# Kernel optimization log

Hardware: AMD Instinct MI355X
Metric: run time of the kernel (lower is better)

## Reference

```python
import jax, jax.numpy as jnp
import numpy as np

N_NODES = 256
DIM = 128
N_LAYERS = 3
LN_EPS = 1e-5


def setup_inputs() -> dict:
    key = jax.random.key(0)
    ks = jax.random.split(key, 8)
    B = 2048
    node_features = jax.random.normal(ks[0], (B, N_NODES, DIM), dtype=jnp.float32)
    A_logits_pos = jax.random.normal(ks[1], (N_NODES, N_NODES), dtype=jnp.float32) * 0.01
    A_logits_neg = jax.random.normal(ks[2], (N_NODES, N_NODES), dtype=jnp.float32) * 0.01
    # per-layer Linear weights, torch layout (out_dim, in_dim); all dims are 128
    scale = 1.0 / np.sqrt(DIM)
    W_pos = jax.random.uniform(ks[3], (N_LAYERS, DIM, DIM), jnp.float32, -scale, scale)
    W_neg = jax.random.uniform(ks[4], (N_LAYERS, DIM, DIM), jnp.float32, -scale, scale)
    ln_g = jnp.ones((N_LAYERS, DIM), jnp.float32)
    ln_b = jnp.zeros((N_LAYERS, DIM), jnp.float32)
    ro_g = jnp.ones((DIM,), jnp.float32)
    ro_b = jnp.zeros((DIM,), jnp.float32)
    return {"node_features": node_features, "A_logits_pos": A_logits_pos,
            "A_logits_neg": A_logits_neg, "W_pos": W_pos, "W_neg": W_neg,
            "ln_g": ln_g, "ln_b": ln_b, "ro_g": ro_g, "ro_b": ro_b}


def _layernorm(x, g, b):
    mu = jnp.mean(x, axis=-1, keepdims=True)
    var = jnp.var(x, axis=-1, keepdims=True)
    return (x - mu) * jax.lax.rsqrt(var + LN_EPS) * g + b


def reference(node_features, A_logits_pos, A_logits_neg, W_pos, W_neg, ln_g, ln_b, ro_g, ro_b):
    # soft signed adjacency with hard-mask split (mask is non-differentiable)
    A_p = jax.nn.sigmoid(A_logits_pos)
    A_n = jax.nn.sigmoid(A_logits_neg)
    mask = (A_p > A_n).astype(A_p.dtype)
    A_pos = A_p * mask
    A_neg = A_n * (1.0 - mask)

    H = node_features  # (B, N, D)
    for l in range(N_LAYERS):
        agg_pos = jnp.einsum('uv,bvd->bud', A_pos, H)
        agg_neg = jnp.einsum('uv,bvd->bud', A_neg, H)
        # torch Linear: x @ W.T ; GELU is exact (erf) by default in torch
        out = jax.nn.gelu(jnp.einsum('bud,od->buo', agg_pos, W_pos[l])
                          - jnp.einsum('bud,od->buo', agg_neg, W_neg[l]),
                          approximate=False)
        H = _layernorm(out, ln_g[l], ln_b[l])  # dropout = identity in eval

    h_G = jnp.mean(H, axis=1)  # (B, D) readout
    return _layernorm(h_G, ro_g, ro_b)
```

## Files before the change

### kernel.cpp

```cpp
#include <hip/hip_runtime.h>
#include <math.h>


typedef float  f32x4  __attribute__((ext_vector_type(4)));
typedef float  f32x16 __attribute__((ext_vector_type(16)));
typedef short  s16x8  __attribute__((ext_vector_type(8)));
typedef __bf16 bf16x8 __attribute__((ext_vector_type(8)));

#define GOFF 65536

__device__ __forceinline__ unsigned short f2bf(float f) {
  unsigned int u = __builtin_bit_cast(unsigned int, f);
  u = (u + 0x7fffu + ((u >> 16) & 1u)) >> 16;
  return (unsigned short)u;
}
__device__ __forceinline__ float bf2f(unsigned short h) {
  return __builtin_bit_cast(float, (unsigned int)h << 16);
}

__device__ __forceinline__ int haddr(int v, int d) {
  return v * 256 + ((d * 2) ^ ((v & 15) << 4));
}
__device__ __forceinline__ int gaddr(int o, int vr) {
  return GOFF + o * 80 + vr * 2;
}

#define MFMA32(a, b, c) __builtin_amdgcn_mfma_f32_32x32x16_bf16( \
    __builtin_bit_cast(bf16x8, (a)), __builtin_bit_cast(bf16x8, (b)), (c), 0, 0, 0)

__global__ void prep_kernel(const float* __restrict__ alp, const float* __restrict__ aln,
                            const float* __restrict__ wp,  const float* __restrict__ wn,
                            unsigned short* __restrict__ A3, unsigned short* __restrict__ W3) {
  int idx = blockIdx.x * 512 + threadIdx.x;
  if (idx < 131072) {
    int j = idx & 7, lane = (idx >> 3) & 63, vt = (idx >> 9) & 15,
        ut = (idx >> 13) & 7, h = (idx >> 16) & 1;
    int u = ut * 32 + (lane & 31);
    int v = vt * 16 + (lane >> 5) * 8 + j;
    int s = u * 256 + v;
    float ap = 1.f / (1.f + expf(-alp[s]));
    float an = 1.f / (1.f + expf(-aln[s]));
    bool  m  = ap > an;
    float val = h ? (m ? 0.f : -an) : (m ? ap : 0.f);
    A3[idx] = f2bf(val);
  } else {
    int k = idx - 131072;
    int j = k & 7, lane = (k >> 3) & 63, kt = (k >> 9) & 7,
        ot = (k >> 12) & 3, hw = (k >> 14);
    int o = ot * 32 + (lane & 31);
    int d = kt * 16 + (lane >> 5) * 8 + j;
    const float* src = (hw & 1) ? wn : wp;
    W3[k] = f2bf(src[(hw >> 1) * 16384 + o * 128 + d]);
  }
}

__global__ __launch_bounds__(256, 2) void gnn_kernel(
    const float* __restrict__ X,
    const unsigned short* __restrict__ A3,
    const unsigned short* __restrict__ W3,
    const float* __restrict__ ln_g, const float* __restrict__ ln_b,
    const float* __restrict__ ro_g, const float* __restrict__ ro_b,
    float* __restrict__ out) {
  extern __shared__ char smem[];
  const int tid  = threadIdx.x;
  const int wid  = tid >> 6;
  const int lane = tid & 63;
  const int l31  = lane & 31;
  const int hi   = lane >> 5;
  const int b    = blockIdx.x;

  {
    const float4* Xb = (const float4*)(X + (size_t)b * 256 * 128);
#pragma unroll 8
    for (int i = 0; i < 32; ++i) {
      int idx = tid + i * 256;
      int v = idx >> 5, d = (idx & 31) * 4;
      float4 f = Xb[idx];
      ushort4 p;
      p.x = f2bf(f.x); p.y = f2bf(f.y); p.z = f2bf(f.z); p.w = f2bf(f.w);
      *(ushort4*)(smem + haddr(v, d)) = p;
    }
  }
  __syncthreads();

  f32x16 acc[2][4];
  for (int l = 0; l < 3; ++l) {
#pragma unroll
    for (int mt = 0; mt < 2; ++mt)
#pragma unroll
      for (int nt = 0; nt < 4; ++nt)
#pragma unroll
        for (int r = 0; r < 16; ++r) acc[mt][nt][r] = 0.f;

    for (int h = 0; h < 2; ++h) {
      const unsigned short* Wb = W3 + (size_t)(((l * 2 + h) * 4 + wid) * 8) * 512;
      const unsigned short* Ab = A3 + (size_t)((h * 8 + wid * 2) * 16) * 512;

      s16x8 wreg[8];
#pragma unroll
      for (int kt = 0; kt < 8; ++kt)
        wreg[kt] = *(const s16x8*)(Wb + (size_t)kt * 512 + lane * 8);

      for (int c = 0; c < 8; ++c) {
        f32x16 g0;
#pragma unroll
        for (int r = 0; r < 16; ++r) g0[r] = 0.f;
        const int v0 = c * 32 + l31;
#pragma unroll
        for (int kt = 0; kt < 8; ++kt) {
          s16x8 ha = *(const s16x8*)(smem + haddr(v0, kt * 16 + hi * 8));
          g0 = MFMA32(ha, wreg[kt], g0);
        }
        __syncthreads();
        {
          const int og = wid * 32 + l31;
#pragma unroll
          for (int rq = 0; rq < 4; ++rq) {
            int vr = rq * 8 + hi * 4;
            ushort4 p;
            p.x = f2bf(g0[rq*4+0]); p.y = f2bf(g0[rq*4+1]);
            p.z = f2bf(g0[rq*4+2]); p.w = f2bf(g0[rq*4+3]);
            *(ushort4*)(smem + gaddr(og, vr)) = p;
          }
        }
        __syncthreads();

#pragma unroll
        for (int kt = 0; kt < 2; ++kt) {
          s16x8 bf[4];
#pragma unroll
          for (int nt = 0; nt < 4; ++nt)
            bf[nt] = *(const s16x8*)(smem + gaddr(nt * 32 + l31, kt * 16 + hi * 8));
          s16x8 a0 = *(const s16x8*)(Ab + (size_t)(0 * 16 + c * 2 + kt) * 512 + lane * 8);
          s16x8 a1 = *(const s16x8*)(Ab + (size_t)(1 * 16 + c * 2 + kt) * 512 + lane * 8);
#pragma unroll
          for (int nt = 0; nt < 4; ++nt) {
            acc[0][nt] = MFMA32(a0, bf[nt], acc[0][nt]);
            acc[1][nt] = MFMA32(a1, bf[nt], acc[1][nt]);
          }
        }
      }
    }

    {
      float lg[4], lb[4];
#pragma unroll
      for (int nt = 0; nt < 4; ++nt) {
        lg[nt] = ln_g[l * 128 + nt * 32 + l31];
        lb[nt] = ln_b[l * 128 + nt * 32 + l31];
      }
#pragma unroll
      for (int mt = 0; mt < 2; ++mt)
#pragma unroll
        for (int r = 0; r < 16; ++r) {
          float x0 = acc[mt][0][r]; x0 = 0.5f * x0 * (1.f + erff(x0 * 0.70710678f));
          float x1 = acc[mt][1][r]; x1 = 0.5f * x1 * (1.f + erff(x1 * 0.70710678f));
          float x2 = acc[mt][2][r]; x2 = 0.5f * x2 * (1.f + erff(x2 * 0.70710678f));
          float x3 = acc[mt][3][r]; x3 = 0.5f * x3 * (1.f + erff(x3 * 0.70710678f));
          acc[mt][0][r] = x0; acc[mt][1][r] = x1;
          acc[mt][2][r] = x2; acc[mt][3][r] = x3;
          float s1 = x0 + x1 + x2 + x3;
          float s2 = x0 * x0 + x1 * x1 + x2 * x2 + x3 * x3;
#pragma unroll
          for (int m = 1; m < 32; m <<= 1) {
            s1 += __shfl_xor(s1, m);
            s2 += __shfl_xor(s2, m);
          }
          float mu  = s1 * (1.f / 128.f);
          float var = s2 * (1.f / 128.f) - mu * mu;
          float rs  = rsqrtf(var + 1e-5f);
          int u = wid * 64 + mt * 32 + (r & 3) + 8 * ((r >> 2) & 3) + 4 * hi;
#pragma unroll
          for (int nt = 0; nt < 4; ++nt) {
            float y = (acc[mt][nt][r] - mu) * rs * lg[nt] + lb[nt];
            *(unsigned short*)(smem + haddr(u, nt * 32 + l31)) = f2bf(y);
          }
        }
    }
    __syncthreads();
  }

  {
    int d   = tid & 127;
    int grp = tid >> 7;
    float s = 0.f;
    for (int v = grp * 128; v < grp * 128 + 128; ++v)
      s += bf2f(*(const unsigned short*)(smem + haddr(v, d)));
    float* red = (float*)(smem + GOFF);
    red[grp * 128 + d] = s;
    __syncthreads();
    if (tid < 128) {
      red[256 + tid] = (red[tid] + red[128 + tid]) * (1.f / 256.f);
    }
    __syncthreads();
    if (tid < 64) {
      float a  = red[256 + tid];
      float b2 = red[256 + 64 + tid];
      float s1 = a + b2, s2 = a * a + b2 * b2;
#pragma unroll
      for (int m = 1; m < 64; m <<= 1) {
        s1 += __shfl_xor(s1, m);
        s2 += __shfl_xor(s2, m);
      }
      float mu  = s1 * (1.f / 128.f);
      float var = s2 * (1.f / 128.f) - mu * mu;
      float rs  = rsqrtf(var + 1e-5f);
      out[(size_t)b * 128 + tid]      = (a  - mu) * rs * ro_g[tid]      + ro_b[tid];
      out[(size_t)b * 128 + 64 + tid] = (b2 - mu) * rs * ro_g[64 + tid] + ro_b[64 + tid];
    }
  }
}

extern "C" void kernel_launch(void* const* d_in, const int* in_sizes, int n_in,
                              void* d_out, int out_size, void* d_ws, size_t ws_size,
                              hipStream_t stream) {
  const float* X   = (const float*)d_in[0];
  const float* alp = (const float*)d_in[1];
  const float* aln = (const float*)d_in[2];
  const float* wp  = (const float*)d_in[3];
  const float* wn  = (const float*)d_in[4];
  const float* lng = (const float*)d_in[5];
  const float* lnb = (const float*)d_in[6];
  const float* rog = (const float*)d_in[7];
  const float* rob = (const float*)d_in[8];
  float* out = (float*)d_out;

  unsigned short* A3 = (unsigned short*)d_ws;
  unsigned short* W3 = A3 + 131072;

  (void)hipFuncSetAttribute(reinterpret_cast<const void*>(gnn_kernel),
                            hipFuncAttributeMaxDynamicSharedMemorySize, 75776);

  prep_kernel<<<448, 512, 0, stream>>>(alp, aln, wp, wn, A3, W3);
  gnn_kernel<<<2048, 256, 75776, stream>>>(X, A3, W3, lng, lnb, rog, rob, out);
}
```

Measured before the change: 701.4 us.

## Keep H·W tile in registers via lane shuffles, restructure waves over output columns

Each wave now owns 32 output feature columns across all 256 nodes, so the H·W intermediate is re-laid out into the MFMA B operand with cross-half-wave shuffles instead of being written to LDS with two block barriers per chunk. The LayerNorm row statistics are combined across waves through a small LDS stats buffer. The fp32-to-bf16 conversion switches to the native cast. In exchange, each wave loads all eight A tiles per chunk from global memory, holds a larger accumulator set, and the LayerNorm pass does more shuffle reductions (one per element) plus an extra barrier.

```diff
diff --git a/kernel.cpp b/kernel.cpp
--- a/kernel.cpp
+++ b/kernel.cpp
@@ -5,24 +5,29 @@
 typedef float  f32x4  __attribute__((ext_vector_type(4)));
 typedef float  f32x16 __attribute__((ext_vector_type(16)));
 typedef short  s16x8  __attribute__((ext_vector_type(8)));
+typedef unsigned int u32x4 __attribute__((ext_vector_type(4)));
 typedef __bf16 bf16x8 __attribute__((ext_vector_type(8)));
 
-#define GOFF 65536
+#define SOFF 65536
 
 __device__ __forceinline__ unsigned short f2bf(float f) {
+  __bf16 h = (__bf16)f;
+  return __builtin_bit_cast(unsigned short, h);
+}
+__device__ __forceinline__ float bf2f(unsigned short h) {
+  return __builtin_bit_cast(float, (unsigned int)h << 16);
+}
+__device__ __forceinline__ unsigned short f2bf_rne(float f) {
   unsigned int u = __builtin_bit_cast(unsigned int, f);
   u = (u + 0x7fffu + ((u >> 16) & 1u)) >> 16;
   return (unsigned short)u;
 }
-__device__ __forceinline__ float bf2f(unsigned short h) {
-  return __builtin_bit_cast(float, (unsigned int)h << 16);
+__device__ __forceinline__ unsigned int pk2(float lo, float hi) {
+  return (unsigned int)f2bf(lo) | ((unsigned int)f2bf(hi) << 16);
 }
 
 __device__ __forceinline__ int haddr(int v, int d) {
   return v * 256 + ((d * 2) ^ ((v & 15) << 4));
-}
-__device__ __forceinline__ int gaddr(int o, int vr) {
-  return GOFF + o * 80 + vr * 2;
 }
 
 #define MFMA32(a, b, c) __builtin_amdgcn_mfma_f32_32x32x16_bf16( \
@@ -42,7 +47,7 @@
     float an = 1.f / (1.f + expf(-aln[s]));
     bool  m  = ap > an;
     float val = h ? (m ? 0.f : -an) : (m ? ap : 0.f);
-    A3[idx] = f2bf(val);
+    A3[idx] = f2bf_rne(val);
   } else {
     int k = idx - 131072;
     int j = k & 7, lane = (k >> 3) & 63, kt = (k >> 9) & 7,
@@ -50,7 +55,7 @@
     int o = ot * 32 + (lane & 31);
     int d = kt * 16 + (lane >> 5) * 8 + j;
     const float* src = (hw & 1) ? wn : wp;
-    W3[k] = f2bf(src[(hw >> 1) * 16384 + o * 128 + d]);
+    W3[k] = f2bf_rne(src[(hw >> 1) * 16384 + o * 128 + d]);
   }
 }
 
@@ -62,12 +67,13 @@
     const float* __restrict__ ro_g, const float* __restrict__ ro_b,
     float* __restrict__ out) {
   extern __shared__ char smem[];
-  const int tid  = threadIdx.x;
-  const int wid  = tid >> 6;
-  const int lane = tid & 63;
-  const int l31  = lane & 31;
-  const int hi   = lane >> 5;
-  const int b    = blockIdx.x;
+  const int  tid  = threadIdx.x;
+  const int  wid  = tid >> 6;
+  const int  lane = tid & 63;
+  const int  l31  = lane & 31;
+  const int  khi  = (lane >> 5) * 8;
+  const bool hib  = lane >= 32;
+  const int  b    = blockIdx.x;
 
   {
     const float4* Xb = (const float4*)(X + (size_t)b * 256 * 128);
@@ -83,100 +89,103 @@
   }
   __syncthreads();
 
-  f32x16 acc[2][4];
+  float* stats = (float*)(smem + SOFF);
+
   for (int l = 0; l < 3; ++l) {
-#pragma unroll
-    for (int mt = 0; mt < 2; ++mt)
-#pragma unroll
-      for (int nt = 0; nt < 4; ++nt)
-#pragma unroll
-        for (int r = 0; r < 16; ++r) acc[mt][nt][r] = 0.f;
+    f32x16 acc[8];
+#pragma unroll
+    for (int ut = 0; ut < 8; ++ut)
+#pragma unroll
+      for (int r = 0; r < 16; ++r) acc[ut][r] = 0.f;
 
     for (int h = 0; h < 2; ++h) {
       const unsigned short* Wb = W3 + (size_t)(((l * 2 + h) * 4 + wid) * 8) * 512;
-      const unsigned short* Ab = A3 + (size_t)((h * 8 + wid * 2) * 16) * 512;
+      const unsigned short* Ab = A3 + (size_t)h * 65536;
 
       s16x8 wreg[8];
 #pragma unroll
       for (int kt = 0; kt < 8; ++kt)
         wreg[kt] = *(const s16x8*)(Wb + (size_t)kt * 512 + lane * 8);
 
+#pragma unroll 1
       for (int c = 0; c < 8; ++c) {
-        f32x16 g0;
-#pragma unroll
-        for (int r = 0; r < 16; ++r) g0[r] = 0.f;
+        f32x16 g;
+#pragma unroll
+        for (int r = 0; r < 16; ++r) g[r] = 0.f;
         const int v0 = c * 32 + l31;
 #pragma unroll
         for (int kt = 0; kt < 8; ++kt) {
-          s16x8 ha = *(const s16x8*)(smem + haddr(v0, kt * 16 + hi * 8));
-          g0 = MFMA32(ha, wreg[kt], g0);
-        }
-        __syncthreads();
-        {
-          const int og = wid * 32 + l31;
-#pragma unroll
-          for (int rq = 0; rq < 4; ++rq) {
-            int vr = rq * 8 + hi * 4;
-            ushort4 p;
-            p.x = f2bf(g0[rq*4+0]); p.y = f2bf(g0[rq*4+1]);
-            p.z = f2bf(g0[rq*4+2]); p.w = f2bf(g0[rq*4+3]);
-            *(ushort4*)(smem + gaddr(og, vr)) = p;
-          }
-        }
-        __syncthreads();
-
-#pragma unroll
-        for (int kt = 0; kt < 2; ++kt) {
-          s16x8 bf[4];
-#pragma unroll
-          for (int nt = 0; nt < 4; ++nt)
-            bf[nt] = *(const s16x8*)(smem + gaddr(nt * 32 + l31, kt * 16 + hi * 8));
-          s16x8 a0 = *(const s16x8*)(Ab + (size_t)(0 * 16 + c * 2 + kt) * 512 + lane * 8);
-          s16x8 a1 = *(const s16x8*)(Ab + (size_t)(1 * 16 + c * 2 + kt) * 512 + lane * 8);
-#pragma unroll
-          for (int nt = 0; nt < 4; ++nt) {
-            acc[0][nt] = MFMA32(a0, bf[nt], acc[0][nt]);
-            acc[1][nt] = MFMA32(a1, bf[nt], acc[1][nt]);
-          }
-        }
-      }
-    }
-
-    {
-      float lg[4], lb[4];
-#pragma unroll
-      for (int nt = 0; nt < 4; ++nt) {
-        lg[nt] = ln_g[l * 128 + nt * 32 + l31];
-        lb[nt] = ln_b[l * 128 + nt * 32 + l31];
-      }
-#pragma unroll
-      for (int mt = 0; mt < 2; ++mt)
-#pragma unroll
-        for (int r = 0; r < 16; ++r) {
-          float x0 = acc[mt][0][r]; x0 = 0.5f * x0 * (1.f + erff(x0 * 0.70710678f));
-          float x1 = acc[mt][1][r]; x1 = 0.5f * x1 * (1.f + erff(x1 * 0.70710678f));
-          float x2 = acc[mt][2][r]; x2 = 0.5f * x2 * (1.f + erff(x2 * 0.70710678f));
-          float x3 = acc[mt][3][r]; x3 = 0.5f * x3 * (1.f + erff(x3 * 0.70710678f));
-          acc[mt][0][r] = x0; acc[mt][1][r] = x1;
-          acc[mt][2][r] = x2; acc[mt][3][r] = x3;
-          float s1 = x0 + x1 + x2 + x3;
-          float s2 = x0 * x0 + x1 * x1 + x2 * x2 + x3 * x3;
-#pragma unroll
-          for (int m = 1; m < 32; m <<= 1) {
-            s1 += __shfl_xor(s1, m);
-            s2 += __shfl_xor(s2, m);
-          }
-          float mu  = s1 * (1.f / 128.f);
+          s16x8 ha = *(const s16x8*)(smem + haddr(v0, kt * 16 + khi));
+          g = MFMA32(ha, wreg[kt], g);
+        }
+        unsigned int w[8], sx[8];
+#pragma unroll
+        for (int i = 0; i < 8; ++i) w[i] = pk2(g[2 * i], g[2 * i + 1]);
+#pragma unroll
+        for (int i = 0; i < 8; ++i)
+          sx[i] = (unsigned int)__shfl_xor((int)w[i], 32);
+        u32x4 fv0 = { hib ? sx[2] : w[0], hib ? sx[3] : w[1],
+                      hib ? w[2] : sx[0], hib ? w[3] : sx[1] };
+        u32x4 fv1 = { hib ? sx[6] : w[4], hib ? sx[7] : w[5],
+                      hib ? w[6] : sx[4], hib ? w[7] : sx[5] };
+        s16x8 bf0 = __builtin_bit_cast(s16x8, fv0);
+        s16x8 bf1 = __builtin_bit_cast(s16x8, fv1);
+
+#pragma unroll
+        for (int ut = 0; ut < 8; ++ut) {
+          s16x8 a0 = *(const s16x8*)(Ab + (size_t)(ut * 16 + c * 2 + 0) * 512 + lane * 8);
+          acc[ut] = MFMA32(a0, bf0, acc[ut]);
+        }
+#pragma unroll
+        for (int ut = 0; ut < 8; ++ut) {
+          s16x8 a1 = *(const s16x8*)(Ab + (size_t)(ut * 16 + c * 2 + 1) * 512 + lane * 8);
+          acc[ut] = MFMA32(a1, bf1, acc[ut]);
+        }
+      }
+    }
+
+    const float lgv = ln_g[l * 128 + wid * 32 + l31];
+    const float lbv = ln_b[l * 128 + wid * 32 + l31];
+#pragma unroll
+    for (int ut = 0; ut < 8; ++ut)
+#pragma unroll
+      for (int r = 0; r < 16; ++r) {
+        float x = acc[ut][r];
+        x = 0.5f * x * (1.f + erff(x * 0.70710678f));
+        acc[ut][r] = x;
+        float s1 = x, s2 = x * x;
+#pragma unroll
+        for (int m = 1; m < 32; m <<= 1) {
+          s1 += __shfl_xor(s1, m);
+          s2 += __shfl_xor(s2, m);
+        }
+        if (l31 == r) {
+          int u = ut * 32 + (r & 3) + 8 * (r >> 2) + (hib ? 4 : 0);
+          float2 pw; pw.x = s1; pw.y = s2;
+          *(float2*)&stats[u * 8 + wid * 2] = pw;
+        }
+      }
+    __syncthreads();
+#pragma unroll
+    for (int ut = 0; ut < 8; ++ut)
+#pragma unroll
+      for (int r = 0; r < 16; ++r) {
+        int u = ut * 32 + (r & 3) + 8 * (r >> 2) + (hib ? 4 : 0);
+        float mu = 0.f, rs = 0.f;
+        if (l31 == r) {
+          f32x4 s01 = *(const f32x4*)&stats[u * 8];
+          f32x4 s23 = *(const f32x4*)&stats[u * 8 + 4];
+          float s1 = s01[0] + s01[2] + s23[0] + s23[2];
+          float s2 = s01[1] + s01[3] + s23[1] + s23[3];
+          mu = s1 * (1.f / 128.f);
           float var = s2 * (1.f / 128.f) - mu * mu;
-          float rs  = rsqrtf(var + 1e-5f);
-          int u = wid * 64 + mt * 32 + (r & 3) + 8 * ((r >> 2) & 3) + 4 * hi;
-#pragma unroll
-          for (int nt = 0; nt < 4; ++nt) {
-            float y = (acc[mt][nt][r] - mu) * rs * lg[nt] + lb[nt];
-            *(unsigned short*)(smem + haddr(u, nt * 32 + l31)) = f2bf(y);
-          }
-        }
-    }
+          rs = rsqrtf(var + 1e-5f);
+        }
+        mu = __shfl(mu, (lane & 32) + r);
+        rs = __shfl(rs, (lane & 32) + r);
+        float y = (acc[ut][r] - mu) * rs * lgv + lbv;
+        *(unsigned short*)(smem + haddr(u, wid * 32 + l31)) = f2bf(y);
+      }
     __syncthreads();
   }
 
@@ -186,7 +195,7 @@
     float s = 0.f;
     for (int v = grp * 128; v < grp * 128 + 128; ++v)
       s += bf2f(*(const unsigned short*)(smem + haddr(v, d)));
-    float* red = (float*)(smem + GOFF);
+    float* red = (float*)(smem + SOFF);
     red[grp * 128 + d] = s;
     __syncthreads();
     if (tid < 128) {
@@ -229,8 +238,8 @@
   unsigned short* W3 = A3 + 131072;
 
   (void)hipFuncSetAttribute(reinterpret_cast<const void*>(gnn_kernel),
-                            hipFuncAttributeMaxDynamicSharedMemorySize, 75776);
+                            hipFuncAttributeMaxDynamicSharedMemorySize, 73728);
 
   prep_kernel<<<448, 512, 0, stream>>>(alp, aln, wp, wn, A3, W3);
-  gnn_kernel<<<2048, 256, 75776, stream>>>(X, A3, W3, lng, lnb, rog, rob, out);
-}
+  gnn_kernel<<<2048, 256, 73728, stream>>>(X, A3, W3, lng, lnb, rog, rob, out);
+}
```

New measurement: 2.404 ms. +242.8%, slower.
